# Performance work log

Hardware: AMD Instinct MI355X
Metric: run time of the kernel (lower is better)

The kernel has to match this reference:

```python
import jax, jax.numpy as jnp
import numpy as np

NUM_ITERATIONS = 3  # init kwarg num_iterations
EPS = 1e-12         # F.normalize eps


def _k_means_routing(priors, num_iterations):
    # priors: (B, O, I, J) = (batch, out_capsules, in_capsules, out_length)
    out = priors.mean(axis=-2, keepdims=True)  # (B, O, 1, J)
    for _ in range(num_iterations):
        norm = jnp.sqrt(jnp.sum(out * out, axis=-1, keepdims=True))
        out_n = out / jnp.maximum(norm, EPS)                       # L2 normalize over J
        logits = jnp.sum(priors * out_n, axis=-1, keepdims=True)   # (B, O, I, 1) dot similarity
        coef = jax.nn.softmax(logits, axis=-2)                     # softmax over in_capsules
        out = jnp.sum(coef * priors, axis=-2, keepdims=True)       # (B, O, 1, J)
    return jnp.squeeze(out, axis=-2)  # (B, O, J); squash=False so no squash


def setup_inputs() -> dict:
    key = jax.random.key(0)
    k1, k2 = jax.random.split(key)
    B, I, L = 32, 512, 64   # batch, in_capsules, in_length
    O, J = 128, 64          # out_capsules, out_length
    x = jax.random.normal(k1, (B, I, L), dtype=jnp.float32)
    # xavier_uniform for weight (O, J, L): fan_in = J*L... torch uses size(1)*prod(rest)
    bound = float(np.sqrt(6.0 / (J * L + O * L)))
    weight = jax.random.uniform(k2, (O, J, L), dtype=jnp.float32, minval=-bound, maxval=bound)
    return {"x": x, "weight": weight}


def reference(x, weight):
    # priors[b,o,i,j] = sum_l weight[o,j,l] * x[b,i,l]  -> (B, O, I, J)
    priors = jnp.einsum('ojl,bil->boij', weight, x)
    return _k_means_routing(priors, NUM_ITERATIONS)
```

## Files before the change

kernel.cpp:

```cpp
#include <hip/hip_runtime.h>
#include <hip/hip_fp16.h>


#define CB 32
#define CI 512
#define CL 64
#define CO 128
#define OPB 16
#define NT 1024

typedef _Float16 half8 __attribute__((ext_vector_type(8)));
typedef float f32x4 __attribute__((ext_vector_type(4)));

static __device__ __forceinline__ _Float16 half_sel(uint v, int sh) {
  union { unsigned short s; _Float16 h; } c;
  c.s = (unsigned short)(v >> sh);
  return c.h;
}

__global__ __launch_bounds__(256) void caps_gram(const float* __restrict__ wg,
                                                 __half2* __restrict__ Gq) {
  const int o = blockIdx.x;
  const int h = blockIdx.y;
  const int t = threadIdx.x;
  __shared__ float wl[64 * 65];
#pragma unroll
  for (int k = 0; k < 16; ++k) {
    int f = t + 256 * k;
    int j = f >> 6, l = f & 63;
    wl[j * 65 + l] = wg[(o << 12) + f];
  }
  __syncthreads();
  const int l1 = h * 32 + (t >> 3);
  const int kq = t & 7;
  const int l2b = kq << 3;
  float acc[8];
#pragma unroll
  for (int m = 0; m < 8; ++m) acc[m] = 0.f;
#pragma unroll 4
  for (int j = 0; j < 64; ++j) {
    float wa = wl[j * 65 + l1];
#pragma unroll
    for (int m = 0; m < 8; ++m) acc[m] += wa * wl[j * 65 + l2b + m];
  }
  union { __half2 h2[4]; uint4 u; } pk;
#pragma unroll
  for (int q = 0; q < 4; ++q)
    pk.h2[q] = __floats2half2_rn(acc[2 * q], acc[2 * q + 1]);
  reinterpret_cast<uint4*>(Gq)[(o << 9) + (kq << 6) + l1] = pk.u;
}

__global__ __launch_bounds__(NT, 4) void caps_main(const float* __restrict__ xg,
                                                   const float* __restrict__ wg,
                                                   const __half2* __restrict__ Gq,
                                                   float* __restrict__ outg) {
  const int b = blockIdx.y;
  const int obase = blockIdx.x * OPB;
  const int t = threadIdx.x;
  const int w = t >> 6;
  const int lane = t & 63;
  const int g = lane >> 4;
  const int o15 = lane & 15;

  __shared__ __align__(16) _Float16 xs[CI * CL];
  __shared__ __align__(16) _Float16 xT[CL * CI];
  __shared__ __align__(16) _Float16 coefT[OPB * CI];
  __shared__ __align__(16) _Float16 wn16[OPB * CL];
  __shared__ __align__(16) float xc_s[OPB * CL];
  __shared__ float se_part[OPB * OPB];
  float* const xcpart = reinterpret_cast<float*>(coefT);
  char* const xs_b = reinterpret_cast<char*>(xs);
  char* const xT_b = reinterpret_cast<char*>(xT);
  char* const cf_b = reinterpret_cast<char*>(coefT);
  char* const wn_b = reinterpret_cast<char*>(wn16);

  const int qh = w >> 2, nt = w & 3;
  const int lcol = nt * 16 + o15;

  const uint4* Gp = reinterpret_cast<const uint4*>(Gq) +
                    ((obase + w) << 9) + lane;
  uint4 ga0, ga1, ga2, ga3;

  {
    const float4* xg4 = reinterpret_cast<const float4*>(xg + b * (CI * CL));
#pragma unroll
    for (int k = 0; k < 4; ++k) {
      int f = t + NT * k;
      int i = f >> 3, lu = f & 7;
      float4 a = xg4[2 * f];
      float4 c = xg4[2 * f + 1];
      union { _Float16 h[8]; uint4 u; } cv;
      cv.h[0] = (_Float16)a.x; cv.h[1] = (_Float16)a.y;
      cv.h[2] = (_Float16)a.z; cv.h[3] = (_Float16)a.w;
      cv.h[4] = (_Float16)c.x; cv.h[5] = (_Float16)c.y;
      cv.h[6] = (_Float16)c.z; cv.h[7] = (_Float16)c.w;
      int off = ((i >> 4) * 4 + (lu >> 1)) * 512 + (i & 15) * 32 + (lu & 1) * 16;
      *reinterpret_cast<uint4*>(xs_b + off) = cv.u;
    }
  }
  __syncthreads();

  {
    const uint* xrd32 = reinterpret_cast<const uint*>(
                            xs_b + nt * 512 + ((o15 & 8) << 1)) +
                        ((o15 & 7) >> 1);
    const int sh = (o15 & 1) << 4;
    float xbs = 0.f;
#define GATHW(K)                                                            \
  {                                                                         \
    int P = qh * 16 + (K)*4 + g;                                            \
    const uint* xk = xrd32 + (P >> 1) * 512 + (P & 1) * 64;                 \
    uint d0 = xk[0], d1 = xk[8], d2 = xk[16], d3 = xk[24];                  \
    uint d4 = xk[32], d5 = xk[40], d6 = xk[48], d7 = xk[56];                \
    union { _Float16 h[8]; uint4 u; } fv;                                   \
    fv.h[0] = half_sel(d0, sh); fv.h[1] = half_sel(d1, sh);                 \
    fv.h[2] = half_sel(d2, sh); fv.h[3] = half_sel(d3, sh);                 \
    fv.h[4] = half_sel(d4, sh); fv.h[5] = half_sel(d5, sh);                 \
    fv.h[6] = half_sel(d6, sh); fv.h[7] = half_sel(d7, sh);                 \
    xbs += (float)fv.h[0] + (float)fv.h[1] + (float)fv.h[2] +               \
           (float)fv.h[3] + (float)fv.h[4] + (float)fv.h[5] +               \
           (float)fv.h[6] + (float)fv.h[7];                                 \
    *reinterpret_cast<uint4*>(xT_b + lcol * 1024 +                          \
                              ((P ^ (lcol & 7)) << 4)) = fv.u;              \
  }
    GATHW(0) GATHW(1) GATHW(2) GATHW(3)
#undef GATHW
    xbs += __shfl_xor(xbs, 16, 64);
    xbs += __shfl_xor(xbs, 32, 64);
    if (lane < 16) xcpart[qh * 1024 + nt * 16 + lane] = xbs;
    ga0 = Gp[0]; ga1 = Gp[64]; ga2 = Gp[128]; ga3 = Gp[192];
  }
  __syncthreads();

  for (int pass = 0; pass < 4; ++pass) {
    if (pass > 0) {
      half8 bw0 = *reinterpret_cast<const half8*>(
          wn_b + o15 * 128 + ((g ^ (o15 & 7)) << 4));
      half8 bw1 = *reinterpret_cast<const half8*>(
          wn_b + o15 * 128 + (((4 + g) ^ (o15 & 7)) << 4));
      float sacc = 0.f;
#pragma unroll
      for (int ti = 0; ti < 2; ++ti) {
        const int st = 2 * w + ti;
        const int itb = st * 2048;
        half8 a0 = *reinterpret_cast<const half8*>(
            xs_b + itb + ((g >> 1) * 512) + o15 * 32 + ((g & 1) << 4));
        half8 a1 = *reinterpret_cast<const half8*>(
            xs_b + itb + ((2 + (g >> 1)) * 512) + o15 * 32 + ((g & 1) << 4));
        f32x4 d = {0.f, 0.f, 0.f, 0.f};
        d = __builtin_amdgcn_mfma_f32_16x16x32_f16(a0, bw0, d, 0, 0, 0);
        d = __builtin_amdgcn_mfma_f32_16x16x32_f16(a1, bw1, d, 0, 0, 0);
        float e0 = __expf(d[0]), e1 = __expf(d[1]);
        float e2 = __expf(d[2]), e3 = __expf(d[3]);
        sacc += (e0 + e1) + (e2 + e3);
        int p = st * 2 + (g >> 1);
        union { _Float16 h[4]; uint2 u; } pk;
        pk.h[0] = (_Float16)e0; pk.h[1] = (_Float16)e1;
        pk.h[2] = (_Float16)e2; pk.h[3] = (_Float16)e3;
        *reinterpret_cast<uint2*>(cf_b + o15 * 1024 + ((p ^ o15) << 4) +
                                  ((g & 1) << 3)) = pk.u;
      }
      if (pass == 3) {
        sacc += __shfl_xor(sacc, 16, 64);
        sacc += __shfl_xor(sacc, 32, 64);
        if (lane < 16) se_part[w * 16 + lane] = sacc;
      }
      __syncthreads();

      if (pass < 3) {
        ga0 = Gp[0]; ga1 = Gp[64]; ga2 = Gp[128]; ga3 = Gp[192];
      }
      f32x4 d = {0.f, 0.f, 0.f, 0.f};
#define MFMAK(K)                                                            \
  {                                                                         \
    int p = qh * 16 + (K)*4 + g;                                            \
    half8 a = *reinterpret_cast<const half8*>(cf_b + o15 * 1024 +           \
                                              ((p ^ o15) << 4));            \
    half8 bv = *reinterpret_cast<const half8*>(xT_b + lcol * 1024 +         \
                                               ((p ^ (lcol & 7)) << 4));    \
    d = __builtin_amdgcn_mfma_f32_16x16x32_f16(a, bv, d, 0, 0, 0);          \
  }
      MFMAK(0) MFMAK(1) MFMAK(2) MFMAK(3)
#undef MFMAK
      __syncthreads();
#pragma unroll
      for (int r = 0; r < 4; ++r)
        xcpart[qh * 1024 + (g * 4 + r) * 64 + lcol] = d[r];
    }
    __syncthreads();

    {
      float sxc;
      if (pass == 0) {
        sxc = xcpart[lane] + xcpart[1024 + lane] + xcpart[2048 + lane] +
              xcpart[3072 + lane];
      } else {
        sxc = xcpart[w * 64 + lane] + xcpart[1024 + w * 64 + lane] +
              xcpart[2048 + w * 64 + lane] + xcpart[3072 + w * 64 + lane];
      }
      float xcv;
      if (pass == 3) {
        float sp = se_part[(lane & 15) * 16 + w];
        sp += __shfl_xor(sp, 1, 64);
        sp += __shfl_xor(sp, 2, 64);
        sp += __shfl_xor(sp, 4, 64);
        sp += __shfl_xor(sp, 8, 64);
        xcv = sxc / sp;
      } else {
        xcv = sxc;
      }
      xc_s[(w << 6) + lane] = xcv;
      if (pass < 3) {
        uint4 gb0 = Gp[256], gb1 = Gp[320], gb2 = Gp[384], gb3 = Gp[448];
        const float4* xc4 = reinterpret_cast<const float4*>(&xc_s[w << 6]);
        float u0 = 0.f, u1 = 0.f, u2 = 0.f, u3 = 0.f;
#define GDOT(V, K)                                                          \
  {                                                                         \
    float4 xa = xc4[2 * (K)], xb = xc4[2 * (K) + 1];                        \
    float2 h0 = __half22float2(*reinterpret_cast<const __half2*>(&V.x));    \
    float2 h1 = __half22float2(*reinterpret_cast<const __half2*>(&V.y));    \
    float2 h2 = __half22float2(*reinterpret_cast<const __half2*>(&V.z));    \
    float2 h3 = __half22float2(*reinterpret_cast<const __half2*>(&V.w));    \
    u0 += h0.x * xa.x; u1 += h0.y * xa.y;                                   \
    u2 += h1.x * xa.z; u3 += h1.y * xa.w;                                   \
    u0 += h2.x * xb.x; u1 += h2.y * xb.y;                                   \
    u2 += h3.x * xb.z; u3 += h3.y * xb.w;                                   \
  }
        GDOT(ga0, 0) GDOT(ga1, 1) GDOT(ga2, 2) GDOT(ga3, 3)
        GDOT(gb0, 4) GDOT(gb1, 5) GDOT(gb2, 6) GDOT(gb3, 7)
#undef GDOT
        float uv = (u0 + u1) + (u2 + u3);
        float sq = uv * xcv;
#pragma unroll
        for (int m = 32; m; m >>= 1) sq += __shfl_xor(sq, m, 64);
        float wnv = uv / fmaxf(sqrtf(fmaxf(sq, 0.f)), 1e-12f);
        union { _Float16 hf; unsigned short us; } wc;
        wc.hf = (_Float16)wnv;
        *reinterpret_cast<unsigned short*>(
            wn_b + w * 128 + (((lane >> 3) ^ (w & 7)) << 4) +
            ((lane & 7) << 1)) = wc.us;
      }
    }
    __syncthreads();
  }

  {
    const float* Wp = wg + ((((obase + w) << 6) + lane) << 6);
    float a0 = 0.f, a1 = 0.f, a2 = 0.f, a3 = 0.f;
#pragma unroll
    for (int k = 0; k < 16; ++k) {
      float4 wv = *reinterpret_cast<const float4*>(&Wp[k << 2]);
      float4 xv = *reinterpret_cast<const float4*>(&xc_s[(w << 6) + (k << 2)]);
      a0 += wv.x * xv.x; a1 += wv.y * xv.y;
      a2 += wv.z * xv.z; a3 += wv.w * xv.w;
    }
    outg[((b << 7) + obase + w) * 64 + lane] = (a0 + a1) + (a2 + a3);
  }
}

extern "C" void kernel_launch(void* const* d_in, const int* in_sizes, int n_in,
                              void* d_out, int out_size, void* d_ws, size_t ws_size,
                              hipStream_t stream) {
  const float* x = (const float*)d_in[0];
  const float* wgt = (const float*)d_in[1];
  float* out = (float*)d_out;
  __half2* Gq = (__half2*)d_ws;

  caps_gram<<<dim3(CO, 2), dim3(256), 0, stream>>>(wgt, Gq);
  caps_main<<<dim3(CO / OPB, CB), dim3(NT), 0, stream>>>(x, wgt, Gq, out);
}
```

Before: 35.18 us.

## Keep x fragments in registers, alias xcpart onto xs, drop a barrier

Loads the phase-A MFMA A-fragments from xs into registers once before the routing loop, so xs can be reused as the xcpart scratch area. That frees coefT from aliasing and lets the barrier between the coef·x MFMA and the xcpart stores be removed. The Gram-matrix prefetch is cut from eight live uint4 registers to a rolling two-at-a-time pipeline, which lowers register pressure. Each interleaved Gram load may now expose more global latency inside the dot product, and removing the barrier depends on xs no longer being read after the initial gather.

```diff
diff --git a/kernel.cpp b/kernel.cpp
--- a/kernel.cpp
+++ b/kernel.cpp
@@ -68,7 +68,7 @@
   __shared__ __align__(16) _Float16 wn16[OPB * CL];
   __shared__ __align__(16) float xc_s[OPB * CL];
   __shared__ float se_part[OPB * OPB];
-  float* const xcpart = reinterpret_cast<float*>(coefT);
+  float* const xcpart = reinterpret_cast<float*>(xs);
   char* const xs_b = reinterpret_cast<char*>(xs);
   char* const xT_b = reinterpret_cast<char*>(xT);
   char* const cf_b = reinterpret_cast<char*>(coefT);
@@ -79,7 +79,7 @@
 
   const uint4* Gp = reinterpret_cast<const uint4*>(Gq) +
                     ((obase + w) << 9) + lane;
-  uint4 ga0, ga1, ga2, ga3;
+  uint4 ga0, ga1;
 
   {
     const float4* xg4 = reinterpret_cast<const float4*>(xg + b * (CI * CL));
@@ -100,12 +100,13 @@
   }
   __syncthreads();
 
+  float xbs = 0.f;
+  half8 af00, af01, af10, af11;
   {
     const uint* xrd32 = reinterpret_cast<const uint*>(
                             xs_b + nt * 512 + ((o15 & 8) << 1)) +
                         ((o15 & 7) >> 1);
     const int sh = (o15 & 1) << 4;
-    float xbs = 0.f;
 #define GATHW(K)                                                            \
   {                                                                         \
     int P = qh * 16 + (K)*4 + g;                                            \
@@ -125,12 +126,17 @@
   }
     GATHW(0) GATHW(1) GATHW(2) GATHW(3)
 #undef GATHW
+    const int abase = (g >> 1) * 512 + o15 * 32 + ((g & 1) << 4);
+    af00 = *reinterpret_cast<const half8*>(xs_b + (2 * w) * 2048 + abase);
+    af01 = *reinterpret_cast<const half8*>(xs_b + (2 * w) * 2048 + 1024 + abase);
+    af10 = *reinterpret_cast<const half8*>(xs_b + (2 * w + 1) * 2048 + abase);
+    af11 = *reinterpret_cast<const half8*>(xs_b + (2 * w + 1) * 2048 + 1024 + abase);
     xbs += __shfl_xor(xbs, 16, 64);
     xbs += __shfl_xor(xbs, 32, 64);
-    if (lane < 16) xcpart[qh * 1024 + nt * 16 + lane] = xbs;
-    ga0 = Gp[0]; ga1 = Gp[64]; ga2 = Gp[128]; ga3 = Gp[192];
+    ga0 = Gp[0]; ga1 = Gp[64];
   }
   __syncthreads();
+  if (lane < 16) xcpart[qh * 1024 + nt * 16 + lane] = xbs;
 
   for (int pass = 0; pass < 4; ++pass) {
     if (pass > 0) {
@@ -139,27 +145,25 @@
       half8 bw1 = *reinterpret_cast<const half8*>(
           wn_b + o15 * 128 + (((4 + g) ^ (o15 & 7)) << 4));
       float sacc = 0.f;
-#pragma unroll
-      for (int ti = 0; ti < 2; ++ti) {
-        const int st = 2 * w + ti;
-        const int itb = st * 2048;
-        half8 a0 = *reinterpret_cast<const half8*>(
-            xs_b + itb + ((g >> 1) * 512) + o15 * 32 + ((g & 1) << 4));
-        half8 a1 = *reinterpret_cast<const half8*>(
-            xs_b + itb + ((2 + (g >> 1)) * 512) + o15 * 32 + ((g & 1) << 4));
-        f32x4 d = {0.f, 0.f, 0.f, 0.f};
-        d = __builtin_amdgcn_mfma_f32_16x16x32_f16(a0, bw0, d, 0, 0, 0);
-        d = __builtin_amdgcn_mfma_f32_16x16x32_f16(a1, bw1, d, 0, 0, 0);
-        float e0 = __expf(d[0]), e1 = __expf(d[1]);
-        float e2 = __expf(d[2]), e3 = __expf(d[3]);
-        sacc += (e0 + e1) + (e2 + e3);
-        int p = st * 2 + (g >> 1);
-        union { _Float16 h[4]; uint2 u; } pk;
-        pk.h[0] = (_Float16)e0; pk.h[1] = (_Float16)e1;
-        pk.h[2] = (_Float16)e2; pk.h[3] = (_Float16)e3;
-        *reinterpret_cast<uint2*>(cf_b + o15 * 1024 + ((p ^ o15) << 4) +
-                                  ((g & 1) << 3)) = pk.u;
-      }
+#define PHASEA(TI, AF0, AF1)                                                \
+  {                                                                         \
+    const int st = 2 * w + (TI);                                            \
+    f32x4 d = {0.f, 0.f, 0.f, 0.f};                                         \
+    d = __builtin_amdgcn_mfma_f32_16x16x32_f16(AF0, bw0, d, 0, 0, 0);       \
+    d = __builtin_amdgcn_mfma_f32_16x16x32_f16(AF1, bw1, d, 0, 0, 0);       \
+    float e0 = __expf(d[0]), e1 = __expf(d[1]);                             \
+    float e2 = __expf(d[2]), e3 = __expf(d[3]);                             \
+    sacc += (e0 + e1) + (e2 + e3);                                          \
+    int p = st * 2 + (g >> 1);                                              \
+    union { _Float16 h[4]; uint2 u; } pk;                                   \
+    pk.h[0] = (_Float16)e0; pk.h[1] = (_Float16)e1;                         \
+    pk.h[2] = (_Float16)e2; pk.h[3] = (_Float16)e3;                         \
+    *reinterpret_cast<uint2*>(cf_b + o15 * 1024 + ((p ^ o15) << 4) +        \
+                              ((g & 1) << 3)) = pk.u;                       \
+  }
+      PHASEA(0, af00, af01)
+      PHASEA(1, af10, af11)
+#undef PHASEA
       if (pass == 3) {
         sacc += __shfl_xor(sacc, 16, 64);
         sacc += __shfl_xor(sacc, 32, 64);
@@ -167,9 +171,6 @@
       }
       __syncthreads();
 
-      if (pass < 3) {
-        ga0 = Gp[0]; ga1 = Gp[64]; ga2 = Gp[128]; ga3 = Gp[192];
-      }
       f32x4 d = {0.f, 0.f, 0.f, 0.f};
 #define MFMAK(K)                                                            \
   {                                                                         \
@@ -182,7 +183,7 @@
   }
       MFMAK(0) MFMAK(1) MFMAK(2) MFMAK(3)
 #undef MFMAK
-      __syncthreads();
+      if (pass < 3) { ga0 = Gp[0]; ga1 = Gp[64]; }
 #pragma unroll
       for (int r = 0; r < 4; ++r)
         xcpart[qh * 1024 + (g * 4 + r) * 64 + lcol] = d[r];
@@ -211,7 +212,6 @@
       }
       xc_s[(w << 6) + lane] = xcv;
       if (pass < 3) {
-        uint4 gb0 = Gp[256], gb1 = Gp[320], gb2 = Gp[384], gb3 = Gp[448];
         const float4* xc4 = reinterpret_cast<const float4*>(&xc_s[w << 6]);
         float u0 = 0.f, u1 = 0.f, u2 = 0.f, u3 = 0.f;
 #define GDOT(V, K)                                                          \
@@ -226,8 +226,13 @@
     u0 += h2.x * xb.x; u1 += h2.y * xb.y;                                   \
     u2 += h3.x * xb.z; u3 += h3.y * xb.w;                                   \
   }
-        GDOT(ga0, 0) GDOT(ga1, 1) GDOT(ga2, 2) GDOT(ga3, 3)
-        GDOT(gb0, 4) GDOT(gb1, 5) GDOT(gb2, 6) GDOT(gb3, 7)
+        uint4 gb0 = Gp[128], gb1 = Gp[192];
+        GDOT(ga0, 0) GDOT(ga1, 1)
+        ga0 = Gp[256]; ga1 = Gp[320];
+        GDOT(gb0, 2) GDOT(gb1, 3)
+        gb0 = Gp[384]; gb1 = Gp[448];
+        GDOT(ga0, 4) GDOT(ga1, 5)
+        GDOT(gb0, 6) GDOT(gb1, 7)
 #undef GDOT
         float uv = (u0 + u1) + (u2 + u3);
         float sq = uv * xcv;
```

Result: faster. 33.05 us (-6.0%).

## Halve output capsules per block and keep transposed x in registers

Applied to the files above, without the earlier changes.

Each block now handles 8 output capsules instead of 16, which doubles the grid. The shared-memory transposed x buffer is dropped: each wave keeps its B-operand fragments in registers, which cuts LDS use and lets more blocks fit per CU (launch bounds raised to 8). The trade-off is that half the MFMA lanes in the 16-wide tiles do redundant work, only 8 waves run the per-capsule normalize and output phases, and x is reloaded and converted twice as often across blocks. Gram-matrix loads are also restructured into a two-stage register prefetch.

```diff
diff --git a/kernel.cpp b/kernel.cpp
--- a/kernel.cpp
+++ b/kernel.cpp
@@ -6,7 +6,7 @@
 #define CI 512
 #define CL 64
 #define CO 128
-#define OPB 16
+#define OPB 8
 #define NT 1024
 
 typedef _Float16 half8 __attribute__((ext_vector_type(8)));
@@ -50,7 +50,7 @@
   reinterpret_cast<uint4*>(Gq)[(o << 9) + (kq << 6) + l1] = pk.u;
 }
 
-__global__ __launch_bounds__(NT, 4) void caps_main(const float* __restrict__ xg,
+__global__ __launch_bounds__(NT, 8) void caps_main(const float* __restrict__ xg,
                                                    const float* __restrict__ wg,
                                                    const __half2* __restrict__ Gq,
                                                    float* __restrict__ outg) {
@@ -61,25 +61,24 @@
   const int lane = t & 63;
   const int g = lane >> 4;
   const int o15 = lane & 15;
+  const int oc = o15 & 7;
 
   __shared__ __align__(16) _Float16 xs[CI * CL];
-  __shared__ __align__(16) _Float16 xT[CL * CI];
-  __shared__ __align__(16) _Float16 coefT[OPB * CI];
+  __shared__ __align__(16) _Float16 cfx[OPB * CI];
   __shared__ __align__(16) _Float16 wn16[OPB * CL];
   __shared__ __align__(16) float xc_s[OPB * CL];
-  __shared__ float se_part[OPB * OPB];
-  float* const xcpart = reinterpret_cast<float*>(coefT);
+  __shared__ float se_part[16 * OPB];
+  float* const xcpart = reinterpret_cast<float*>(cfx);
   char* const xs_b = reinterpret_cast<char*>(xs);
-  char* const xT_b = reinterpret_cast<char*>(xT);
-  char* const cf_b = reinterpret_cast<char*>(coefT);
+  char* const cf_b = reinterpret_cast<char*>(cfx);
   char* const wn_b = reinterpret_cast<char*>(wn16);
 
   const int qh = w >> 2, nt = w & 3;
   const int lcol = nt * 16 + o15;
 
   const uint4* Gp = reinterpret_cast<const uint4*>(Gq) +
-                    ((obase + w) << 9) + lane;
-  uint4 ga0, ga1, ga2, ga3;
+                    ((obase + (w & 7)) << 9) + lane;
+  uint4 ga0, ga1;
 
   {
     const float4* xg4 = reinterpret_cast<const float4*>(xg + b * (CI * CL));
@@ -100,13 +99,14 @@
   }
   __syncthreads();
 
+  uint4 bt0, bt1, bt2, bt3;
+  float xbs = 0.f;
   {
     const uint* xrd32 = reinterpret_cast<const uint*>(
                             xs_b + nt * 512 + ((o15 & 8) << 1)) +
                         ((o15 & 7) >> 1);
     const int sh = (o15 & 1) << 4;
-    float xbs = 0.f;
-#define GATHW(K)                                                            \
+#define GATHW(K, BT)                                                        \
   {                                                                         \
     int P = qh * 16 + (K)*4 + g;                                            \
     const uint* xk = xrd32 + (P >> 1) * 512 + (P & 1) * 64;                 \
@@ -120,87 +120,88 @@
     xbs += (float)fv.h[0] + (float)fv.h[1] + (float)fv.h[2] +               \
            (float)fv.h[3] + (float)fv.h[4] + (float)fv.h[5] +               \
            (float)fv.h[6] + (float)fv.h[7];                                 \
-    *reinterpret_cast<uint4*>(xT_b + lcol * 1024 +                          \
-                              ((P ^ (lcol & 7)) << 4)) = fv.u;              \
-  }
-    GATHW(0) GATHW(1) GATHW(2) GATHW(3)
+    BT = fv.u;                                                              \
+  }
+    GATHW(0, bt0) GATHW(1, bt1) GATHW(2, bt2) GATHW(3, bt3)
 #undef GATHW
     xbs += __shfl_xor(xbs, 16, 64);
     xbs += __shfl_xor(xbs, 32, 64);
-    if (lane < 16) xcpart[qh * 1024 + nt * 16 + lane] = xbs;
-    ga0 = Gp[0]; ga1 = Gp[64]; ga2 = Gp[128]; ga3 = Gp[192];
+    if (g == 0) xcpart[qh * 512 + lcol] = xbs;
+    if (w < 8) { ga0 = Gp[0]; ga1 = Gp[64]; }
   }
   __syncthreads();
 
   for (int pass = 0; pass < 4; ++pass) {
     if (pass > 0) {
       half8 bw0 = *reinterpret_cast<const half8*>(
-          wn_b + o15 * 128 + ((g ^ (o15 & 7)) << 4));
+          wn_b + oc * 128 + ((g ^ oc) << 4));
       half8 bw1 = *reinterpret_cast<const half8*>(
-          wn_b + o15 * 128 + (((4 + g) ^ (o15 & 7)) << 4));
+          wn_b + oc * 128 + (((4 + g) ^ oc) << 4));
       float sacc = 0.f;
 #pragma unroll
       for (int ti = 0; ti < 2; ++ti) {
         const int st = 2 * w + ti;
         const int itb = st * 2048;
+        const int abase = o15 * 32 + ((g & 1) << 4);
         half8 a0 = *reinterpret_cast<const half8*>(
-            xs_b + itb + ((g >> 1) * 512) + o15 * 32 + ((g & 1) << 4));
+            xs_b + itb + ((g >> 1) * 512) + abase);
         half8 a1 = *reinterpret_cast<const half8*>(
-            xs_b + itb + ((2 + (g >> 1)) * 512) + o15 * 32 + ((g & 1) << 4));
+            xs_b + itb + ((2 + (g >> 1)) * 512) + abase);
         f32x4 d = {0.f, 0.f, 0.f, 0.f};
         d = __builtin_amdgcn_mfma_f32_16x16x32_f16(a0, bw0, d, 0, 0, 0);
         d = __builtin_amdgcn_mfma_f32_16x16x32_f16(a1, bw1, d, 0, 0, 0);
         float e0 = __expf(d[0]), e1 = __expf(d[1]);
         float e2 = __expf(d[2]), e3 = __expf(d[3]);
         sacc += (e0 + e1) + (e2 + e3);
-        int p = st * 2 + (g >> 1);
-        union { _Float16 h[4]; uint2 u; } pk;
-        pk.h[0] = (_Float16)e0; pk.h[1] = (_Float16)e1;
-        pk.h[2] = (_Float16)e2; pk.h[3] = (_Float16)e3;
-        *reinterpret_cast<uint2*>(cf_b + o15 * 1024 + ((p ^ o15) << 4) +
-                                  ((g & 1) << 3)) = pk.u;
+        if (o15 < 8) {
+          int p = st * 2 + (g >> 1);
+          union { _Float16 h[4]; uint2 u; } pk;
+          pk.h[0] = (_Float16)e0; pk.h[1] = (_Float16)e1;
+          pk.h[2] = (_Float16)e2; pk.h[3] = (_Float16)e3;
+          *reinterpret_cast<uint2*>(cf_b + o15 * 1024 + ((p ^ o15) << 4) +
+                                    ((g & 1) << 3)) = pk.u;
+        }
       }
       if (pass == 3) {
         sacc += __shfl_xor(sacc, 16, 64);
         sacc += __shfl_xor(sacc, 32, 64);
-        if (lane < 16) se_part[w * 16 + lane] = sacc;
+        if (lane < 8) se_part[w * 8 + lane] = sacc;
       }
       __syncthreads();
 
-      if (pass < 3) {
-        ga0 = Gp[0]; ga1 = Gp[64]; ga2 = Gp[128]; ga3 = Gp[192];
-      }
+      if (w < 8 && pass < 3) { ga0 = Gp[0]; ga1 = Gp[64]; }
       f32x4 d = {0.f, 0.f, 0.f, 0.f};
-#define MFMAK(K)                                                            \
+#define MFMAK(K, BT)                                                        \
   {                                                                         \
     int p = qh * 16 + (K)*4 + g;                                            \
-    half8 a = *reinterpret_cast<const half8*>(cf_b + o15 * 1024 +           \
-                                              ((p ^ o15) << 4));            \
-    half8 bv = *reinterpret_cast<const half8*>(xT_b + lcol * 1024 +         \
-                                               ((p ^ (lcol & 7)) << 4));    \
-    d = __builtin_amdgcn_mfma_f32_16x16x32_f16(a, bv, d, 0, 0, 0);          \
-  }
-      MFMAK(0) MFMAK(1) MFMAK(2) MFMAK(3)
+    half8 a = *reinterpret_cast<const half8*>(cf_b + oc * 1024 +            \
+                                              ((p ^ oc) << 4));             \
+    d = __builtin_amdgcn_mfma_f32_16x16x32_f16(                             \
+        a, *reinterpret_cast<const half8*>(&BT), d, 0, 0, 0);               \
+  }
+      MFMAK(0, bt0) MFMAK(1, bt1) MFMAK(2, bt2) MFMAK(3, bt3)
 #undef MFMAK
       __syncthreads();
-#pragma unroll
-      for (int r = 0; r < 4; ++r)
-        xcpart[qh * 1024 + (g * 4 + r) * 64 + lcol] = d[r];
-    }
-    __syncthreads();
-
-    {
+      if (g < 2) {
+#pragma unroll
+        for (int r = 0; r < 4; ++r)
+          xcpart[qh * 512 + (g * 4 + r) * 64 + lcol] = d[r];
+      }
+      __syncthreads();
+    }
+
+    if (w < 8) {
       float sxc;
       if (pass == 0) {
-        sxc = xcpart[lane] + xcpart[1024 + lane] + xcpart[2048 + lane] +
-              xcpart[3072 + lane];
+        sxc = xcpart[lane] + xcpart[512 + lane] + xcpart[1024 + lane] +
+              xcpart[1536 + lane];
       } else {
-        sxc = xcpart[w * 64 + lane] + xcpart[1024 + w * 64 + lane] +
-              xcpart[2048 + w * 64 + lane] + xcpart[3072 + w * 64 + lane];
+        sxc = xcpart[w * 64 + lane] + xcpart[512 + w * 64 + lane] +
+              xcpart[1024 + w * 64 + lane] + xcpart[1536 + w * 64 + lane];
       }
       float xcv;
       if (pass == 3) {
-        float sp = se_part[(lane & 15) * 16 + w];
+        float sp = se_part[(lane & 15) * 8 + w];
         sp += __shfl_xor(sp, 1, 64);
         sp += __shfl_xor(sp, 2, 64);
         sp += __shfl_xor(sp, 4, 64);
@@ -211,7 +212,6 @@
       }
       xc_s[(w << 6) + lane] = xcv;
       if (pass < 3) {
-        uint4 gb0 = Gp[256], gb1 = Gp[320], gb2 = Gp[384], gb3 = Gp[448];
         const float4* xc4 = reinterpret_cast<const float4*>(&xc_s[w << 6]);
         float u0 = 0.f, u1 = 0.f, u2 = 0.f, u3 = 0.f;
 #define GDOT(V, K)                                                          \
@@ -226,8 +226,13 @@
     u0 += h2.x * xb.x; u1 += h2.y * xb.y;                                   \
     u2 += h3.x * xb.z; u3 += h3.y * xb.w;                                   \
   }
-        GDOT(ga0, 0) GDOT(ga1, 1) GDOT(ga2, 2) GDOT(ga3, 3)
-        GDOT(gb0, 4) GDOT(gb1, 5) GDOT(gb2, 6) GDOT(gb3, 7)
+        uint4 gb0 = Gp[128], gb1 = Gp[192];
+        GDOT(ga0, 0) GDOT(ga1, 1)
+        ga0 = Gp[256]; ga1 = Gp[320];
+        GDOT(gb0, 2) GDOT(gb1, 3)
+        gb0 = Gp[384]; gb1 = Gp[448];
+        GDOT(ga0, 4) GDOT(ga1, 5)
+        GDOT(gb0, 6) GDOT(gb1, 7)
 #undef GDOT
         float uv = (u0 + u1) + (u2 + u3);
         float sq = uv * xcv;
@@ -237,14 +242,14 @@
         union { _Float16 hf; unsigned short us; } wc;
         wc.hf = (_Float16)wnv;
         *reinterpret_cast<unsigned short*>(
-            wn_b + w * 128 + (((lane >> 3) ^ (w & 7)) << 4) +
-            ((lane & 7) << 1)) = wc.us;
+            wn_b + w * 128 + (((lane >> 3) ^ w) << 4) + ((lane & 7) << 1)) =
+            wc.us;
       }
     }
     __syncthreads();
   }
 
-  {
+  if (w < 8) {
     const float* Wp = wg + ((((obase + w) << 6) + lane) << 6);
     float a0 = 0.f, a1 = 0.f, a2 = 0.f, a3 = 0.f;
 #pragma unroll
```

New measurement: 73.12 us. +107.9%, slower.
